# Kernel tuning notes

Measured on AMD Instinct MI355X. Metric: run time of the kernel, lower is better.

## Reference

```python
import jax, jax.numpy as jnp
import numpy as np

N_HEADS = 12

def setup_inputs() -> dict:
    key = jax.random.key(0)
    ks = jax.random.split(key, 6)
    B, S, C = 8, 1024, 768
    x = jax.random.normal(ks[0], (B, S, C), dtype=jnp.float32)
    attention_mask = jnp.ones((B, S), dtype=jnp.int32)
    scale = 1.0 / np.sqrt(C)
    w_qkv = jax.random.normal(ks[1], (3 * C, C), dtype=jnp.float32) * scale
    b_qkv = jnp.zeros((3 * C,), dtype=jnp.float32)
    w_out = jax.random.normal(ks[2], (C, C), dtype=jnp.float32) * scale
    b_out = jnp.zeros((C,), dtype=jnp.float32)
    return {"x": x, "w_qkv": w_qkv, "b_qkv": b_qkv, "w_out": w_out,
            "b_out": b_out, "attention_mask": attention_mask}


def reference(x, w_qkv, b_qkv, w_out, b_out, attention_mask):
    B, S, C = x.shape
    H = N_HEADS
    D = C // H
    qkv = x @ w_qkv.T + b_qkv                      # [B,S,3C]
    q, k, v = jnp.split(qkv, 3, axis=2)
    # [B,S,C] -> [B,H,S,D]
    q = q.reshape(B, S, H, D).transpose(0, 2, 1, 3)
    k = k.reshape(B, S, H, D).transpose(0, 2, 1, 3)
    v = v.reshape(B, S, H, D).transpose(0, 2, 1, 3)
    att = jnp.einsum('bhsd,bhtd->bhst', q, k) / np.sqrt(D).astype(jnp.float32)
    causal = jnp.tril(jnp.ones((S, S), dtype=bool))[None, None]      # [1,1,S,S]
    key_mask = attention_mask.astype(bool)[:, None, None, :]        # [B,1,1,S]
    mask = causal & key_mask                                        # [B,1,S,S]
    neg = jnp.finfo(att.dtype).min
    att = jnp.where(mask, att, neg)
    att = jax.nn.softmax(att, axis=-1)
    att = jnp.where(mask, att, 0.0)                                 # second masked_fill
    y = jnp.einsum('bhst,bhtd->bhsd', att, v)                       # [B,H,S,D]
    y = y.transpose(0, 2, 1, 3).reshape(B, S, C)
    return y @ w_out.T + b_out
```

## Files before the change

### kernel.cpp

```cpp
#include <hip/hip_runtime.h>
#include <hip/hip_bf16.h>
#include <math.h>

#define BATCH 8
#define SEQ   1024
#define CDIM  768
#define NH    12
#define HD    64
#define M_TOT (BATCH * SEQ)
#define N_QKV (3 * CDIM)
#define KDIM  768

typedef __attribute__((ext_vector_type(4))) _Float16 half4;
typedef __attribute__((ext_vector_type(8))) _Float16 half8;
typedef __attribute__((ext_vector_type(4))) float floatx4;

__device__ __forceinline__ void gld_lds16(const _Float16* g, _Float16* l) {
    __builtin_amdgcn_global_load_lds(
        (const __attribute__((address_space(1))) void*)g,
        (__attribute__((address_space(3))) void*)l, 16, 0, 0);
}

__device__ __forceinline__ float exp2_fast(float x) {
#if __has_builtin(__builtin_amdgcn_exp2f)
    return __builtin_amdgcn_exp2f(x);
#else
    float r; asm("v_exp_f32 %0, %1" : "=v"(r) : "v"(x)); return r;
#endif
}

__global__ __launch_bounds__(256) void cvt_all(
    const float* __restrict__ x, const float* __restrict__ wq,
    const float* __restrict__ wo,
    _Float16* __restrict__ x16, _Float16* __restrict__ wq16,
    _Float16* __restrict__ wo16)
{
    const int bid = blockIdx.x;
    const float* src; _Float16* dst; size_t base;
    if (bid < 6144)      { src = x;  dst = x16;  base = (size_t)bid * 1024; }
    else if (bid < 7872) { src = wq; dst = wq16; base = (size_t)(bid - 6144) * 1024; }
    else                 { src = wo; dst = wo16; base = (size_t)(bid - 7872) * 1024; }
    const size_t i = base + threadIdx.x * 4;
    float4 v = *reinterpret_cast<const float4*>(src + i);
    half4 h;
    h[0] = (_Float16)v.x; h[1] = (_Float16)v.y;
    h[2] = (_Float16)v.z; h[3] = (_Float16)v.w;
    *reinterpret_cast<half4*>(dst + i) = h;
}

__global__ __launch_bounds__(256) void gemm_qkv(
    const _Float16* __restrict__ A, const _Float16* __restrict__ B,
    const float* __restrict__ bias, _Float16* __restrict__ C,
    _Float16* __restrict__ VT)
{
    __shared__ _Float16 Atile[128 * 64];
    __shared__ _Float16 Btile[128 * 64];
    const int tid  = threadIdx.x;
    const int wave = tid >> 6, lane = tid & 63, quad = lane >> 4, l16 = lane & 15;
    const int wm = wave >> 1, wn = wave & 1;
    const int m0 = blockIdx.y * 128, n0 = blockIdx.x * 128;

    const int strow = tid >> 3;
    const int scg   = (tid & 7) ^ (strow & 7);
    const _Float16* gA = A + (size_t)(m0 + strow) * KDIM + scg * 8;
    const _Float16* gB = B + (size_t)(n0 + strow) * KDIM + scg * 8;
    _Float16* lA = Atile + tid * 8;
    _Float16* lB = Btile + tid * 8;

    floatx4 acc[4][4];
#pragma unroll
    for (int i = 0; i < 4; ++i)
#pragma unroll
        for (int j = 0; j < 4; ++j) acc[i][j] = (floatx4){0.f, 0.f, 0.f, 0.f};

    for (int k0 = 0; k0 < KDIM; k0 += 64) {
        __syncthreads();
#pragma unroll
        for (int i = 0; i < 4; ++i) {
            gld_lds16(gA + (size_t)(i * 32) * KDIM + k0, lA + i * 2048);
            gld_lds16(gB + (size_t)(i * 32) * KDIM + k0, lB + i * 2048);
        }
        __syncthreads();
#pragma unroll
        for (int kk = 0; kk < 2; ++kk) {
            const int cg = (quad + kk * 4) ^ (l16 & 7);
            half8 aF[4], bF[4];
#pragma unroll
            for (int mt = 0; mt < 4; ++mt)
                aF[mt] = *reinterpret_cast<const half8*>(
                    &Atile[(wm * 64 + mt * 16 + l16) * 64 + cg * 8]);
#pragma unroll
            for (int nt = 0; nt < 4; ++nt)
                bF[nt] = *reinterpret_cast<const half8*>(
                    &Btile[(wn * 64 + nt * 16 + l16) * 64 + cg * 8]);
#pragma unroll
            for (int mt = 0; mt < 4; ++mt)
#pragma unroll
                for (int nt = 0; nt < 4; ++nt)
                    acc[mt][nt] = __builtin_amdgcn_mfma_f32_16x16x32_f16(
                        aF[mt], bF[nt], acc[mt][nt], 0, 0, 0);
        }
    }

    if (n0 < 2 * CDIM) {
#pragma unroll
        for (int nt = 0; nt < 4; ++nt) {
            const int col = n0 + wn * 64 + nt * 16 + l16;
            const float bv = bias[col];
#pragma unroll
            for (int mt = 0; mt < 4; ++mt) {
                const int rowb = m0 + wm * 64 + mt * 16 + quad * 4;
#pragma unroll
                for (int r = 0; r < 4; ++r)
                    C[(size_t)(rowb + r) * N_QKV + col] = (_Float16)(acc[mt][nt][r] + bv);
            }
        }
    } else {
        const int bb = m0 >> 10;
#pragma unroll
        for (int nt = 0; nt < 4; ++nt) {
            const int colf = n0 + wn * 64 + nt * 16 + l16;
            const float bv = bias[colf];
            const int hd = colf - 2 * CDIM;
            const int hh = hd >> 6, d = hd & 63;
#pragma unroll
            for (int mt = 0; mt < 4; ++mt) {
                const int rowb = m0 + wm * 64 + mt * 16 + quad * 4;
                const int s = rowb & 1023;
                half4 hv;
#pragma unroll
                for (int r = 0; r < 4; ++r) hv[r] = (_Float16)(acc[mt][nt][r] + bv);
                *reinterpret_cast<half4*>(
                    &VT[((size_t)(bb * NH + hh) * HD + d) * SEQ + s]) = hv;
            }
        }
    }
}

__global__ __launch_bounds__(256) void gemm_out(
    const _Float16* __restrict__ A, const _Float16* __restrict__ B,
    const float* __restrict__ bias, float* __restrict__ C)
{
    __shared__ _Float16 Atile[64 * 64];
    __shared__ _Float16 Btile[128 * 64];
    const int tid  = threadIdx.x;
    const int wave = tid >> 6, lane = tid & 63, quad = lane >> 4, l16 = lane & 15;
    const int m0 = blockIdx.y * 64, n0 = blockIdx.x * 128;

    const int strow = tid >> 3;
    const int scg   = (tid & 7) ^ (strow & 7);
    const _Float16* gA = A + (size_t)(m0 + strow) * KDIM + scg * 8;
    const _Float16* gB = B + (size_t)(n0 + strow) * KDIM + scg * 8;
    _Float16* lA = Atile + tid * 8;
    _Float16* lB = Btile + tid * 8;

    floatx4 acc[8];
#pragma unroll
    for (int i = 0; i < 8; ++i) acc[i] = (floatx4){0.f, 0.f, 0.f, 0.f};

    for (int k0 = 0; k0 < KDIM; k0 += 64) {
        __syncthreads();
        gld_lds16(gA + k0, lA);
        gld_lds16(gA + (size_t)32 * KDIM + k0, lA + 2048);
#pragma unroll
        for (int i = 0; i < 4; ++i)
            gld_lds16(gB + (size_t)(i * 32) * KDIM + k0, lB + i * 2048);
        __syncthreads();
#pragma unroll
        for (int kk = 0; kk < 2; ++kk) {
            const int cg = (quad + kk * 4) ^ (l16 & 7);
            half8 aF = *reinterpret_cast<const half8*>(
                &Atile[(wave * 16 + l16) * 64 + cg * 8]);
            half8 bF[8];
#pragma unroll
            for (int nt = 0; nt < 8; ++nt)
                bF[nt] = *reinterpret_cast<const half8*>(
                    &Btile[(nt * 16 + l16) * 64 + cg * 8]);
#pragma unroll
            for (int nt = 0; nt < 8; ++nt)
                acc[nt] = __builtin_amdgcn_mfma_f32_16x16x32_f16(
                    aF, bF[nt], acc[nt], 0, 0, 0);
        }
    }

#pragma unroll
    for (int nt = 0; nt < 8; ++nt) {
        const int col = n0 + nt * 16 + l16;
        const float bv = bias[col];
        const int rowb = m0 + wave * 16 + quad * 4;
#pragma unroll
        for (int r = 0; r < 4; ++r)
            C[(size_t)(rowb + r) * CDIM + col] = acc[nt][r] + bv;
    }
}

__global__ __launch_bounds__(256) void flash_attn(
    const _Float16* __restrict__ QKV, const _Float16* __restrict__ VT,
    const int* __restrict__ amask, _Float16* __restrict__ Y)
{
    __shared__ __align__(16) char smraw[32768];
    _Float16 (*Klds)[4096] = (_Float16 (*)[4096])smraw;
    _Float16 (*Vlds)[4096] = (_Float16 (*)[4096])(smraw + 16384);
    _Float16 (*osm)[72]    = (_Float16 (*)[72])smraw;

    const int qt = blockIdx.x, h = blockIdx.y, b = blockIdx.z;
    const int tid = threadIdx.x;
    const int w = tid >> 6, lane = tid & 63, quad = lane >> 4, l16 = lane & 15;
    const int qbA = qt * 64, qbB = (15 - qt) * 64;
    int qi[2] = { qbA + w * 16 + l16, qbB + w * 16 + l16 };

    const _Float16 qscale = (_Float16)0.18033688f;
    half8 qf[2][2];
#pragma unroll
    for (int qg = 0; qg < 2; ++qg)
#pragma unroll
        for (int kc = 0; kc < 2; ++kc) {
            half8 q = *reinterpret_cast<const half8*>(
                QKV + (size_t)(b * SEQ + qi[qg]) * N_QKV + h * HD + kc * 32 + quad * 8);
#pragma unroll
            for (int i = 0; i < 8; ++i) q[i] = q[i] * qscale;
            qf[qg][kc] = q;
        }

    float rsum[2] = {0.f, 0.f};
    floatx4 accO[2][4];
#pragma unroll
    for (int qg = 0; qg < 2; ++qg)
#pragma unroll
        for (int dt = 0; dt < 4; ++dt) accO[qg][dt] = (floatx4){0.f, 0.f, 0.f, 0.f};

    const int srow0 = w * 16 + (lane >> 3);
    const int scg   = ((lane & 7) ^ (srow0 & 7)) * 8;
    const _Float16* gK = QKV + ((size_t)b * SEQ + srow0) * N_QKV + CDIM + h * HD + scg;
    const _Float16* gV = VT + ((size_t)(b * NH + h) * HD + srow0) * SEQ + scg;

    const int nt = 16 - qt;

    gld_lds16(gK,             &Klds[0][w * 1024]);
    gld_lds16(gK + 8 * N_QKV, &Klds[0][w * 1024 + 512]);
    gld_lds16(gV,             &Vlds[0][w * 1024]);
    gld_lds16(gV + 8 * SEQ,   &Vlds[0][w * 1024 + 512]);
    int4 mcur[4];
#pragma unroll
    for (int kt = 0; kt < 4; ++kt)
        mcur[kt] = *reinterpret_cast<const int4*>(&amask[b * SEQ + kt * 16 + quad * 4]);

    for (int t = 0; t < nt; ++t) {
        const int buf = t & 1, nbuf = buf ^ 1;
        const int t0 = t * 64;
        const bool actA = (t <= qt), fullA = (t < qt), fullB = (t + qt < 15);

        __syncthreads();

        int4 mnext[4];
        if (t + 1 < nt) {
            const int t1 = t0 + 64;
            gld_lds16(gK + (size_t)t1 * N_QKV,       &Klds[nbuf][w * 1024]);
            gld_lds16(gK + (size_t)(t1 + 8) * N_QKV, &Klds[nbuf][w * 1024 + 512]);
            gld_lds16(gV + t1,                       &Vlds[nbuf][w * 1024]);
            gld_lds16(gV + t1 + 8 * SEQ,             &Vlds[nbuf][w * 1024 + 512]);
#pragma unroll
            for (int kt = 0; kt < 4; ++kt)
                mnext[kt] = *reinterpret_cast<const int4*>(
                    &amask[b * SEQ + t1 + kt * 16 + quad * 4]);
        }

        float bias[4][4];
#pragma unroll
        for (int kt = 0; kt < 4; ++kt) {
            bias[kt][0] = mcur[kt].x ? 0.f : -1e30f;
            bias[kt][1] = mcur[kt].y ? 0.f : -1e30f;
            bias[kt][2] = mcur[kt].z ? 0.f : -1e30f;
            bias[kt][3] = mcur[kt].w ? 0.f : -1e30f;
        }

        half4 pfA[4], pfB[4];
#pragma unroll
        for (int kt = 0; kt < 4; ++kt) {
            floatx4 aS0 = (floatx4){0.f, 0.f, 0.f, 0.f};
            floatx4 aS1 = (floatx4){0.f, 0.f, 0.f, 0.f};
            const int krow = kt * 16 + l16;
#pragma unroll
            for (int kc = 0; kc < 2; ++kc) {
                half8 kf = *reinterpret_cast<const half8*>(
                    &Klds[buf][krow * 64 + (((kc * 4 + quad) ^ (krow & 7)) * 8)]);
                if (actA) aS0 = __builtin_amdgcn_mfma_f32_16x16x32_f16(kf, qf[0][kc], aS0, 0, 0, 0);
                aS1 = __builtin_amdgcn_mfma_f32_16x16x32_f16(kf, qf[1][kc], aS1, 0, 0, 0);
            }
            float pA[4], pB[4];
#pragma unroll
            for (int r = 0; r < 4; ++r) {
                const int key = t0 + kt * 16 + quad * 4 + r;
                float sB = aS1[r] + bias[kt][r];
                if (!fullB && key > qi[1]) sB = -1e30f;
                pB[r] = exp2_fast(sB);
                if (actA) {
                    float sA = aS0[r] + bias[kt][r];
                    if (!fullA && key > qi[0]) sA = -1e30f;
                    pA[r] = exp2_fast(sA);
                }
            }
            rsum[1] += (pB[0] + pB[1]) + (pB[2] + pB[3]);
            {
                auto lo = __builtin_amdgcn_cvt_pkrtz(pB[0], pB[1]);
                auto hi = __builtin_amdgcn_cvt_pkrtz(pB[2], pB[3]);
                half4 pf; pf[0] = lo[0]; pf[1] = lo[1]; pf[2] = hi[0]; pf[3] = hi[1];
                pfB[kt] = pf;
            }
            if (actA) {
                rsum[0] += (pA[0] + pA[1]) + (pA[2] + pA[3]);
                auto lo = __builtin_amdgcn_cvt_pkrtz(pA[0], pA[1]);
                auto hi = __builtin_amdgcn_cvt_pkrtz(pA[2], pA[3]);
                half4 pf; pf[0] = lo[0]; pf[1] = lo[1]; pf[2] = hi[0]; pf[3] = hi[1];
                pfA[kt] = pf;
            }
        }

#pragma unroll
        for (int dt = 0; dt < 4; ++dt) {
            const int vrow = dt * 16 + l16;
#pragma unroll
            for (int kt = 0; kt < 4; ++kt) {
                half4 vf = *reinterpret_cast<const half4*>(
                    &Vlds[buf][vrow * 64 +
                               (((kt * 2 + (quad >> 1)) ^ (vrow & 7)) * 8) +
                               (quad & 1) * 4]);
                if (actA) accO[0][dt] = __builtin_amdgcn_mfma_f32_16x16x16f16(
                    vf, pfA[kt], accO[0][dt], 0, 0, 0);
                accO[1][dt] = __builtin_amdgcn_mfma_f32_16x16x16f16(
                    vf, pfB[kt], accO[1][dt], 0, 0, 0);
            }
        }

        if (t + 1 < nt) {
#pragma unroll
            for (int kt = 0; kt < 4; ++kt) mcur[kt] = mnext[kt];
        }
    }

    float inv[2];
#pragma unroll
    for (int qg = 0; qg < 2; ++qg) {
        float l = rsum[qg];
        l += __shfl_xor(l, 16, 64);
        l += __shfl_xor(l, 32, 64);
        inv[qg] = (l > 0.f) ? 1.f / l : 0.f;
    }

    __syncthreads();
#pragma unroll
    for (int qg = 0; qg < 2; ++qg)
#pragma unroll
        for (int dt = 0; dt < 4; ++dt)
#pragma unroll
            for (int r = 0; r < 4; ++r)
                osm[qg * 64 + w * 16 + l16][dt * 16 + quad * 4 + r] =
                    (_Float16)(accO[qg][dt][r] * inv[qg]);
    __syncthreads();

    const int q  = tid >> 1;
    const int dc = (tid & 1) * 32;
    const int grow = (q < 64) ? (qbA + q) : (qbB + q - 64);
    _Float16* dst = Y + ((size_t)(b * SEQ + grow)) * CDIM + h * HD + dc;
#pragma unroll
    for (int i = 0; i < 4; ++i)
        *reinterpret_cast<half8*>(dst + 8 * i) =
            *reinterpret_cast<const half8*>(&osm[q][dc + 8 * i]);
}

extern "C" void kernel_launch(void* const* d_in, const int* in_sizes, int n_in,
                              void* d_out, int out_size, void* d_ws, size_t ws_size,
                              hipStream_t stream)
{
    const float* x      = (const float*)d_in[0];
    const float* w_qkv  = (const float*)d_in[1];
    const float* b_qkv  = (const float*)d_in[2];
    const float* w_out  = (const float*)d_in[3];
    const float* b_out  = (const float*)d_in[4];
    const int*   amask  = (const int*)d_in[5];
    float* out = (float*)d_out;

    _Float16* ws = (_Float16*)d_ws;
    _Float16* x16    = ws;
    _Float16* wqkv16 = x16 + (size_t)M_TOT * CDIM;
    _Float16* wout16 = wqkv16 + (size_t)N_QKV * CDIM;
    _Float16* qkv16  = wout16 + (size_t)CDIM * CDIM;
    _Float16* y16    = qkv16 + (size_t)M_TOT * N_QKV;
    _Float16* VT     = y16 + (size_t)M_TOT * CDIM;

    cvt_all<<<8448, 256, 0, stream>>>(x, w_qkv, w_out, x16, wqkv16, wout16);

    gemm_qkv<<<dim3(N_QKV / 128, M_TOT / 128), 256, 0, stream>>>(
        x16, wqkv16, b_qkv, qkv16, VT);
    flash_attn<<<dim3(8, NH, BATCH), 256, 0, stream>>>(
        qkv16, VT, amask, y16);
    gemm_out<<<dim3(CDIM / 128, M_TOT / 64), 256, 0, stream>>>(
        y16, wout16, b_out, out);
}
```

Baseline: 200.3 us.

## Double-buffer LDS tiles in QKV and output GEMMs with K-step 32

Both projection GEMMs now use two LDS buffers with a K-tile of 32 instead of a single buffer with a K-tile of 64. The next tile is prefetched through global_load_lds while the current one is consumed, leaving one barrier per iteration instead of two. The LDS swizzle is adapted to the 32-element row width. This is meant to hide global-load latency behind MFMA work, at the cost of twice as many loop iterations, each with less compute to cover the barrier.

```diff
diff --git a/kernel.cpp b/kernel.cpp
--- a/kernel.cpp
+++ b/kernel.cpp
@@ -48,24 +48,23 @@
     *reinterpret_cast<half4*>(dst + i) = h;
 }
 
+#define NKIT (KDIM / 32)
 __global__ __launch_bounds__(256) void gemm_qkv(
     const _Float16* __restrict__ A, const _Float16* __restrict__ B,
     const float* __restrict__ bias, _Float16* __restrict__ C,
     _Float16* __restrict__ VT)
 {
-    __shared__ _Float16 Atile[128 * 64];
-    __shared__ _Float16 Btile[128 * 64];
+    __shared__ _Float16 Atile[2][128 * 32];
+    __shared__ _Float16 Btile[2][128 * 32];
     const int tid  = threadIdx.x;
     const int wave = tid >> 6, lane = tid & 63, quad = lane >> 4, l16 = lane & 15;
     const int wm = wave >> 1, wn = wave & 1;
     const int m0 = blockIdx.y * 128, n0 = blockIdx.x * 128;
 
-    const int strow = tid >> 3;
-    const int scg   = (tid & 7) ^ (strow & 7);
+    const int strow = tid >> 2;
+    const int scg   = (tid & 3) ^ ((strow >> 2) & 3);
     const _Float16* gA = A + (size_t)(m0 + strow) * KDIM + scg * 8;
     const _Float16* gB = B + (size_t)(n0 + strow) * KDIM + scg * 8;
-    _Float16* lA = Atile + tid * 8;
-    _Float16* lB = Btile + tid * 8;
 
     floatx4 acc[4][4];
 #pragma unroll
@@ -73,33 +72,38 @@
 #pragma unroll
         for (int j = 0; j < 4; ++j) acc[i][j] = (floatx4){0.f, 0.f, 0.f, 0.f};
 
-    for (int k0 = 0; k0 < KDIM; k0 += 64) {
+    gld_lds16(gA,                    Atile[0] + tid * 8);
+    gld_lds16(gA + (size_t)64 * KDIM, Atile[0] + 2048 + tid * 8);
+    gld_lds16(gB,                    Btile[0] + tid * 8);
+    gld_lds16(gB + (size_t)64 * KDIM, Btile[0] + 2048 + tid * 8);
+
+    const int rchunk = quad ^ (l16 >> 2);
+
+    for (int kt = 0; kt < NKIT; ++kt) {
+        const int buf = kt & 1;
         __syncthreads();
-#pragma unroll
-        for (int i = 0; i < 4; ++i) {
-            gld_lds16(gA + (size_t)(i * 32) * KDIM + k0, lA + i * 2048);
-            gld_lds16(gB + (size_t)(i * 32) * KDIM + k0, lB + i * 2048);
-        }
-        __syncthreads();
-#pragma unroll
-        for (int kk = 0; kk < 2; ++kk) {
-            const int cg = (quad + kk * 4) ^ (l16 & 7);
-            half8 aF[4], bF[4];
-#pragma unroll
-            for (int mt = 0; mt < 4; ++mt)
-                aF[mt] = *reinterpret_cast<const half8*>(
-                    &Atile[(wm * 64 + mt * 16 + l16) * 64 + cg * 8]);
+        if (kt + 1 < NKIT) {
+            const int k1 = (kt + 1) * 32;
+            gld_lds16(gA + k1,                         Atile[buf ^ 1] + tid * 8);
+            gld_lds16(gA + (size_t)64 * KDIM + k1,     Atile[buf ^ 1] + 2048 + tid * 8);
+            gld_lds16(gB + k1,                         Btile[buf ^ 1] + tid * 8);
+            gld_lds16(gB + (size_t)64 * KDIM + k1,     Btile[buf ^ 1] + 2048 + tid * 8);
+        }
+        half8 aF[4], bF[4];
+#pragma unroll
+        for (int mt = 0; mt < 4; ++mt)
+            aF[mt] = *reinterpret_cast<const half8*>(
+                &Atile[buf][(wm * 64 + mt * 16 + l16) * 32 + rchunk * 8]);
+#pragma unroll
+        for (int nt = 0; nt < 4; ++nt)
+            bF[nt] = *reinterpret_cast<const half8*>(
+                &Btile[buf][(wn * 64 + nt * 16 + l16) * 32 + rchunk * 8]);
+#pragma unroll
+        for (int mt = 0; mt < 4; ++mt)
 #pragma unroll
             for (int nt = 0; nt < 4; ++nt)
-                bF[nt] = *reinterpret_cast<const half8*>(
-                    &Btile[(wn * 64 + nt * 16 + l16) * 64 + cg * 8]);
-#pragma unroll
-            for (int mt = 0; mt < 4; ++mt)
-#pragma unroll
-                for (int nt = 0; nt < 4; ++nt)
-                    acc[mt][nt] = __builtin_amdgcn_mfma_f32_16x16x32_f16(
-                        aF[mt], bF[nt], acc[mt][nt], 0, 0, 0);
-        }
+                acc[mt][nt] = __builtin_amdgcn_mfma_f32_16x16x32_f16(
+                    aF[mt], bF[nt], acc[mt][nt], 0, 0, 0);
     }
 
     if (n0 < 2 * CDIM) {
@@ -141,46 +145,47 @@
     const _Float16* __restrict__ A, const _Float16* __restrict__ B,
     const float* __restrict__ bias, float* __restrict__ C)
 {
-    __shared__ _Float16 Atile[64 * 64];
-    __shared__ _Float16 Btile[128 * 64];
+    __shared__ _Float16 Atile[2][64 * 32];
+    __shared__ _Float16 Btile[2][128 * 32];
     const int tid  = threadIdx.x;
     const int wave = tid >> 6, lane = tid & 63, quad = lane >> 4, l16 = lane & 15;
     const int m0 = blockIdx.y * 64, n0 = blockIdx.x * 128;
 
-    const int strow = tid >> 3;
-    const int scg   = (tid & 7) ^ (strow & 7);
+    const int strow = tid >> 2;
+    const int scg   = (tid & 3) ^ ((strow >> 2) & 3);
     const _Float16* gA = A + (size_t)(m0 + strow) * KDIM + scg * 8;
     const _Float16* gB = B + (size_t)(n0 + strow) * KDIM + scg * 8;
-    _Float16* lA = Atile + tid * 8;
-    _Float16* lB = Btile + tid * 8;
 
     floatx4 acc[8];
 #pragma unroll
     for (int i = 0; i < 8; ++i) acc[i] = (floatx4){0.f, 0.f, 0.f, 0.f};
 
-    for (int k0 = 0; k0 < KDIM; k0 += 64) {
+    gld_lds16(gA,                     Atile[0] + tid * 8);
+    gld_lds16(gB,                     Btile[0] + tid * 8);
+    gld_lds16(gB + (size_t)64 * KDIM, Btile[0] + 2048 + tid * 8);
+
+    const int rchunk = quad ^ (l16 >> 2);
+
+    for (int kt = 0; kt < NKIT; ++kt) {
+        const int buf = kt & 1;
         __syncthreads();
-        gld_lds16(gA + k0, lA);
-        gld_lds16(gA + (size_t)32 * KDIM + k0, lA + 2048);
-#pragma unroll
-        for (int i = 0; i < 4; ++i)
-            gld_lds16(gB + (size_t)(i * 32) * KDIM + k0, lB + i * 2048);
-        __syncthreads();
-#pragma unroll
-        for (int kk = 0; kk < 2; ++kk) {
-            const int cg = (quad + kk * 4) ^ (l16 & 7);
-            half8 aF = *reinterpret_cast<const half8*>(
-                &Atile[(wave * 16 + l16) * 64 + cg * 8]);
-            half8 bF[8];
-#pragma unroll
-            for (int nt = 0; nt < 8; ++nt)
-                bF[nt] = *reinterpret_cast<const half8*>(
-                    &Btile[(nt * 16 + l16) * 64 + cg * 8]);
-#pragma unroll
-            for (int nt = 0; nt < 8; ++nt)
-                acc[nt] = __builtin_amdgcn_mfma_f32_16x16x32_f16(
-                    aF, bF[nt], acc[nt], 0, 0, 0);
-        }
+        if (kt + 1 < NKIT) {
+            const int k1 = (kt + 1) * 32;
+            gld_lds16(gA + k1,                         Atile[buf ^ 1] + tid * 8);
+            gld_lds16(gB + k1,                         Btile[buf ^ 1] + tid * 8);
+            gld_lds16(gB + (size_t)64 * KDIM + k1,     Btile[buf ^ 1] + 2048 + tid * 8);
+        }
+        half8 aF = *reinterpret_cast<const half8*>(
+            &Atile[buf][(wave * 16 + l16) * 32 + rchunk * 8]);
+        half8 bF[8];
+#pragma unroll
+        for (int nt = 0; nt < 8; ++nt)
+            bF[nt] = *reinterpret_cast<const half8*>(
+                &Btile[buf][(nt * 16 + l16) * 32 + rchunk * 8]);
+#pragma unroll
+        for (int nt = 0; nt < 8; ++nt)
+            acc[nt] = __builtin_amdgcn_mfma_f32_16x16x32_f16(
+                aF, bF[nt], acc[nt], 0, 0, 0);
     }
 
 #pragma unroll
```

Result: slower. 215.5 us (+7.6%).
